# Kernel optimization log

Hardware: AMD Instinct MI355X
Metric: run time of the kernel (lower is better)

Reference implementation:

```python
import jax, jax.numpy as jnp
import numpy as np

H, W, DIM, B, K = 28, 28, 384, 64, 1
EPS = 1e-5


def setup_inputs() -> dict:
    key = jax.random.key(0)
    k1, k2, k3 = jax.random.split(key, 3)
    L = 1 + K * H * W
    x = jax.random.normal(k1, (B, L, DIM), dtype=jnp.float32)
    w_reduction = jax.random.normal(k2, (2 * DIM, 4 * DIM), dtype=jnp.float32) * 0.02
    w_convert = jax.random.normal(k3, (2 * DIM, DIM), dtype=jnp.float32) * 0.02
    ln_gamma = jnp.ones((4 * DIM,), dtype=jnp.float32)
    ln_beta = jnp.zeros((4 * DIM,), dtype=jnp.float32)
    return {"x": x, "w_reduction": w_reduction, "w_convert": w_convert,
            "ln_gamma": ln_gamma, "ln_beta": ln_beta}


def reference(x, w_reduction, w_convert, ln_gamma, ln_beta):
    Bb, L, C = x.shape
    k = (L - 1) // (H * W)
    cls_token = x[:, 0:1, :]                      # [B,1,C]
    feat = x[:, 1:, :].reshape(Bb, k, H, W, C)
    x0 = feat[:, :, 0::2, 0::2, :]                # [B,k,H/2,W/2,C]
    x1 = feat[:, :, 1::2, 0::2, :]
    x2 = feat[:, :, 0::2, 1::2, :]
    x3 = feat[:, :, 1::2, 1::2, :]
    m = jnp.concatenate([x0, x1, x2, x3], axis=-1)  # [B,k,H/2,W/2,4C]
    m = m.reshape(Bb, k, -1, 4 * C)
    # LayerNorm over last dim
    mu = jnp.mean(m, axis=-1, keepdims=True)
    var = jnp.mean(jnp.square(m - mu), axis=-1, keepdims=True)
    m = (m - mu) * jax.lax.rsqrt(var + EPS) * ln_gamma + ln_beta
    red = jnp.einsum('bknf,of->bkno', m, w_reduction).reshape(Bb, -1, 2 * C)
    cls_out = jnp.einsum('bic,oc->bio', cls_token, w_convert)  # [B,1,2C]
    return jnp.concatenate([cls_out, red], axis=1)
```

## Files before the change

### kernel.cpp

```cpp
#include <hip/hip_runtime.h>
#include <hip/hip_bf16.h>

#define DIMC 384
#define LL 785
#define FDIM 1536
#define ODIM 768
#define NPATCH 196
#define MROWS 12544
#define BATCH 64

typedef __attribute__((ext_vector_type(8))) short bf16x8;
typedef __attribute__((ext_vector_type(4))) float floatx4;
typedef __attribute__((ext_vector_type(4))) unsigned short ushort4v;

#define WS_WBF_OFF  38535168
#define WS_PST_OFF  40894464
#define WS_B2_OFF   41295872

#define PB_CLS   0
#define PB_CAST  192
#define PB_BIAS  1760
#define PB_WBF   1952
#define PREP_BLOCKS 3104

__device__ __forceinline__ unsigned short f2bf(float f) {
  union { float f; unsigned int u; } v; v.f = f;
  unsigned int u = v.u + 0x7fffu + ((v.u >> 16) & 1u);
  return (unsigned short)(u >> 16);
}

__device__ __forceinline__ void gload_lds16(const void* g, void* l) {
  __builtin_amdgcn_global_load_lds(
      (const __attribute__((address_space(1))) unsigned int*)g,
      (__attribute__((address_space(3))) unsigned int*)l, 16, 0, 0);
}

__global__ __launch_bounds__(256) void prep_kernel(
    const float* __restrict__ x, const float* __restrict__ wred,
    const float* __restrict__ wconv, const float* __restrict__ gamma,
    const float* __restrict__ beta, unsigned short* __restrict__ xbf,
    unsigned short* __restrict__ wbf, float2* __restrict__ pst,
    float2* __restrict__ bias2, float* __restrict__ out) {
  const int blk = blockIdx.x;
  const int t = threadIdx.x;
  const int wv = t >> 6;
  const int lane = t & 63;

  if (blk >= PB_CAST && blk < PB_BIAS) {
    const int w = (blk - PB_CAST) * 4 + wv;
    const int vid0 = w * 8 + (lane >> 4) * 2;
    const int sub = lane & 15;
    float4 v[2][6];
    float s[2], s2[2];
#pragma unroll
    for (int r = 0; r < 2; ++r) {
      int vid = vid0 + r;
      int b = vid / 784;
      int ll = vid - b * 784;
      const float* src = x + ((size_t)b * LL + 1 + ll) * DIMC;
      s[r] = 0.f; s2[r] = 0.f;
#pragma unroll
      for (int c = 0; c < 6; ++c) {
        float4 vv = *reinterpret_cast<const float4*>(src + sub * 4 + c * 64);
        v[r][c] = vv;
        s[r]  += vv.x + vv.y + vv.z + vv.w;
        s2[r] += vv.x * vv.x + vv.y * vv.y + vv.z * vv.z + vv.w * vv.w;
      }
    }
#pragma unroll
    for (int r = 0; r < 2; ++r) {
      unsigned short* dst = xbf + (size_t)(vid0 + r) * DIMC;
#pragma unroll
      for (int c = 0; c < 6; ++c) {
        float4 vv = v[r][c];
        union { ushort4v u4; __hip_bfloat162 h[2]; } u;
        u.h[0] = __float22bfloat162_rn(make_float2(vv.x, vv.y));
        u.h[1] = __float22bfloat162_rn(make_float2(vv.z, vv.w));
        *reinterpret_cast<ushort4v*>(dst + sub * 4 + c * 64) = u.u4;
      }
    }
#pragma unroll
    for (int o = 1; o < 16; o <<= 1) {
#pragma unroll
      for (int r = 0; r < 2; ++r) {
        s[r]  += __shfl_xor(s[r], o);
        s2[r] += __shfl_xor(s2[r], o);
      }
    }
    if (sub == 0) {
      float4 pp = make_float4(s[0], s2[0], s[1], s2[1]);
      *reinterpret_cast<float4*>(&pst[vid0]) = pp;
    }
  } else if (blk < PB_CAST) {
    __shared__ float xs[DIMC];
    int idx = blk;
    int b = idx / 3;
    int ch = idx - b * 3;
    for (int c = t; c < DIMC; c += 256) xs[c] = x[(size_t)b * LL * DIMC + c];
    __syncthreads();
    int o = ch * 256 + t;
    const float* wr = wconv + (size_t)o * DIMC;
    float a0 = 0.f, a1 = 0.f;
#pragma unroll 4
    for (int c = 0; c < DIMC; c += 8) {
      float4 w0 = *reinterpret_cast<const float4*>(wr + c);
      float4 w1 = *reinterpret_cast<const float4*>(wr + c + 4);
      float4 p0 = *reinterpret_cast<const float4*>(&xs[c]);
      float4 p1 = *reinterpret_cast<const float4*>(&xs[c + 4]);
      a0 += w0.x * p0.x + w0.y * p0.y + w0.z * p0.z + w0.w * p0.w;
      a1 += w1.x * p1.x + w1.y * p1.y + w1.z * p1.z + w1.w * p1.w;
    }
    out[(size_t)b * 197 * ODIM + o] = a0 + a1;
  } else if (blk < PB_WBF) {
    int o = (blk - PB_BIAS) * 4 + wv;
    const float* wr = wred + (size_t)o * FDIM;
    float sb = 0.f, sg = 0.f;
#pragma unroll
    for (int c = 0; c < 6; ++c) {
      int f = lane * 4 + c * 256;
      float4 w = *reinterpret_cast<const float4*>(wr + f);
      float4 be = *reinterpret_cast<const float4*>(beta + f);
      float4 ga = *reinterpret_cast<const float4*>(gamma + f);
      sb += w.x * be.x + w.y * be.y + w.z * be.z + w.w * be.w;
      sg += w.x * ga.x + w.y * ga.y + w.z * ga.z + w.w * ga.w;
    }
#pragma unroll
    for (int o2 = 32; o2 > 0; o2 >>= 1) {
      sb += __shfl_down(sb, o2);
      sg += __shfl_down(sg, o2);
    }
    if (lane == 0) bias2[o] = make_float2(sg, sb);
  } else {
    int idx4 = (blk - PB_WBF) * 256 + t;
    int e0 = idx4 * 4;
    int f = e0 % FDIM;
    float4 w = *reinterpret_cast<const float4*>(wred + e0);
    float4 g = *reinterpret_cast<const float4*>(gamma + f);
    ushort4v u;
    u.x = f2bf(w.x * g.x); u.y = f2bf(w.y * g.y);
    u.z = f2bf(w.z * g.z); u.w = f2bf(w.w * g.w);
    *reinterpret_cast<ushort4v*>(wbf + e0) = u;
  }
}

__global__ __launch_bounds__(256) void gemm_kernel(
    const unsigned short* __restrict__ xbf,
    const unsigned short* __restrict__ wbf,
    const float2* __restrict__ pst, const float2* __restrict__ bias2,
    float* __restrict__ out) {
  __shared__ unsigned short As[2][64 * 64];
  __shared__ unsigned short Bs[2][64 * 64];
  __shared__ float2 st[128];

  const int t = threadIdx.x;

  const int NWG = (ODIM / 128) * (MROWS / 128);
  const int qq = NWG >> 3, rr = NWG & 7;
  int bid = blockIdx.x;
  int xcd = bid & 7, pos = bid >> 3;
  int wg = (xcd < rr) ? xcd * (qq + 1) + pos
                      : rr * (qq + 1) + (xcd - rr) * qq + pos;
  int my = wg / 6;
  int nx = wg - my * 6;
  const int mBase = my * 128;
  const int nBase = nx * 128;

  if (t < 128) {
    int m = mBase + t;
    int b = m / NPATCH;
    int n = m - b * NPATCH;
    int i = n / 14;
    int j = n - i * 14;
    int base = b * 784 + i * 56 + j * 2;
    float2 p0 = pst[base];
    float2 p1 = pst[base + 28];
    float2 p2 = pst[base + 1];
    float2 p3 = pst[base + 29];
    float s = p0.x + p1.x + p2.x + p3.x;
    float s2 = p0.y + p1.y + p2.y + p3.y;
    float mu = s * (1.f / FDIM);
    float var = s2 * (1.f / FDIM) - mu * mu;
    float rs = rsqrtf(var + 1e-5f);
    st[t] = make_float2(rs, -mu * rs);
  }

  const unsigned short* agp[2];
  const unsigned short* bgp[2];
  unsigned int ldso[2];
#pragma unroll
  for (int p = 0; p < 2; ++p) {
    int s = p * 256 + t;
    int rho = s >> 3;
    int g = (s & 7) ^ (rho & 7);
    int r = rho + ((g >> 2) << 6);
    int kc = g & 3;
    int m = mBase + r;
    int b = m / NPATCH;
    int n = m - b * NPATCH;
    int i = n / 14;
    int j = n - i * 14;
    agp[p] = xbf + ((size_t)b * 784 + i * 56 + j * 2) * DIMC + kc * 8;
    bgp[p] = wbf + (size_t)(nBase + r) * FDIM + kc * 8;
    ldso[p] = (unsigned)s * 8;
  }

  const int wv = t >> 6;
  const int lane = t & 63;
  const int ln15 = lane & 15;
  const int quad = lane >> 4;
  const int wm = wv >> 1;
  const int wn = wv & 1;

  unsigned int aoff[4], boff[4];
#pragma unroll
  for (int mt = 0; mt < 4; ++mt) {
    int rho = mt * 16 + ln15;
    aoff[mt] = (unsigned)(rho * 64 + (((wm * 4 + quad) ^ (rho & 7)) * 8));
    boff[mt] = (unsigned)(rho * 64 + (((wn * 4 + quad) ^ (rho & 7)) * 8));
  }

  floatx4 acc[4][4];
#pragma unroll
  for (int mt = 0; mt < 4; ++mt)
#pragma unroll
    for (int nt = 0; nt < 4; ++nt)
      acc[mt][nt] = floatx4{0.f, 0.f, 0.f, 0.f};

#pragma unroll
  for (int p = 0; p < 2; ++p) {
    gload_lds16(agp[p], &As[0][ldso[p]]);
    gload_lds16(bgp[p], &Bs[0][ldso[p]]);
  }
  __syncthreads();

  int nq = 0, nkk = 0;
  for (int kt = 0; kt < FDIM / 32; ++kt) {
    const int cur = kt & 1;
    if (kt + 1 < FDIM / 32) {
      if (++nkk == 12) { nkk = 0; ++nq; }
      int ao = ((nq & 1) * 28 + ((nq >> 1) & 1)) * DIMC + nkk * 32;
#pragma unroll
      for (int p = 0; p < 2; ++p) {
        gload_lds16(agp[p] + ao, &As[cur ^ 1][ldso[p]]);
        bgp[p] += 32;
        gload_lds16(bgp[p], &Bs[cur ^ 1][ldso[p]]);
      }
    }
    bf16x8 af[4], bfr[4];
#pragma unroll
    for (int mt = 0; mt < 4; ++mt)
      af[mt] = *reinterpret_cast<const bf16x8*>(&As[cur][aoff[mt]]);
#pragma unroll
    for (int nt = 0; nt < 4; ++nt)
      bfr[nt] = *reinterpret_cast<const bf16x8*>(&Bs[cur][boff[nt]]);
#pragma unroll
    for (int mt = 0; mt < 4; ++mt)
#pragma unroll
      for (int nt = 0; nt < 4; ++nt)
        acc[mt][nt] = __builtin_amdgcn_mfma_f32_16x16x32_bf16(
            af[mt], bfr[nt], acc[mt][nt], 0, 0, 0);
    __syncthreads();
  }

  float2 gb[4];
#pragma unroll
  for (int nt = 0; nt < 4; ++nt)
    gb[nt] = bias2[nBase + wn * 64 + nt * 16 + ln15];
#pragma unroll
  for (int mt = 0; mt < 4; ++mt) {
#pragma unroll
    for (int r = 0; r < 4; ++r) {
      int rloc = wm * 64 + mt * 16 + quad * 4 + r;
      float2 sn = st[rloc];
      int m = mBase + rloc;
      int b = m / NPATCH;
      int n = m - b * NPATCH;
      float* orow = out + ((size_t)b * 197 + 1 + n) * ODIM + nBase + wn * 64;
#pragma unroll
      for (int nt = 0; nt < 4; ++nt) {
        float val = fmaf(acc[mt][nt][r], sn.x,
                         fmaf(sn.y, gb[nt].x, gb[nt].y));
        __builtin_nontemporal_store(val, &orow[nt * 16 + ln15]);
      }
    }
  }
}

extern "C" void kernel_launch(void* const* d_in, const int* in_sizes, int n_in,
                              void* d_out, int out_size, void* d_ws, size_t ws_size,
                              hipStream_t stream) {
  const float* x     = (const float*)d_in[0];
  const float* wred  = (const float*)d_in[1];
  const float* wconv = (const float*)d_in[2];
  const float* gamma = (const float*)d_in[3];
  const float* beta  = (const float*)d_in[4];
  float* out = (float*)d_out;

  unsigned short* xbf = (unsigned short*)d_ws;
  unsigned short* wbf = (unsigned short*)((char*)d_ws + WS_WBF_OFF);
  float2* pst         = (float2*)((char*)d_ws + WS_PST_OFF);
  float2* bias2       = (float2*)((char*)d_ws + WS_B2_OFF);

  prep_kernel<<<dim3(PREP_BLOCKS), 256, 0, stream>>>(x, wred, wconv, gamma,
                                                     beta, xbf, wbf, pst,
                                                     bias2, out);
  gemm_kernel<<<dim3((ODIM / 128) * (MROWS / 128)), 256, 0, stream>>>(
      xbf, wbf, pst, bias2, out);
}
```

Measured before the change: 196.6 us.

## Load GEMM weight fragments directly to registers and deepen K-step to 64

The weight (B) operand is no longer staged through shared memory. Each lane now loads its MFMA B fragments straight from global memory into registers, double-buffered across K steps. The A tile in LDS is enlarged to a 128x64 K-slice, which halves the number of K iterations and barriers. This removes the B-side LDS traffic and half of the synchronisation, at the cost of more VGPRs for the register-held B fragments and less coalesced global reads for the weights.

```diff
diff --git a/kernel.cpp b/kernel.cpp
--- a/kernel.cpp
+++ b/kernel.cpp
@@ -148,8 +148,7 @@
     const unsigned short* __restrict__ wbf,
     const float2* __restrict__ pst, const float2* __restrict__ bias2,
     float* __restrict__ out) {
-  __shared__ unsigned short As[2][64 * 64];
-  __shared__ unsigned short Bs[2][64 * 64];
+  __shared__ unsigned short As[2][128 * 64];
   __shared__ float2 st[128];
 
   const int t = threadIdx.x;
@@ -184,23 +183,19 @@
     st[t] = make_float2(rs, -mu * rs);
   }
 
-  const unsigned short* agp[2];
-  const unsigned short* bgp[2];
-  unsigned int ldso[2];
-#pragma unroll
-  for (int p = 0; p < 2; ++p) {
+  const unsigned short* agp[4];
+  unsigned int ldso[4];
+#pragma unroll
+  for (int p = 0; p < 4; ++p) {
     int s = p * 256 + t;
-    int rho = s >> 3;
-    int g = (s & 7) ^ (rho & 7);
-    int r = rho + ((g >> 2) << 6);
-    int kc = g & 3;
+    int r = s >> 3;
+    int cs = (s & 7) ^ (r & 7);
     int m = mBase + r;
     int b = m / NPATCH;
     int n = m - b * NPATCH;
     int i = n / 14;
     int j = n - i * 14;
-    agp[p] = xbf + ((size_t)b * 784 + i * 56 + j * 2) * DIMC + kc * 8;
-    bgp[p] = wbf + (size_t)(nBase + r) * FDIM + kc * 8;
+    agp[p] = xbf + ((size_t)b * 784 + i * 56 + j * 2) * DIMC + cs * 8;
     ldso[p] = (unsigned)s * 8;
   }
 
@@ -211,13 +206,20 @@
   const int wm = wv >> 1;
   const int wn = wv & 1;
 
-  unsigned int aoff[4], boff[4];
-#pragma unroll
-  for (int mt = 0; mt < 4; ++mt) {
-    int rho = mt * 16 + ln15;
-    aoff[mt] = (unsigned)(rho * 64 + (((wm * 4 + quad) ^ (rho & 7)) * 8));
-    boff[mt] = (unsigned)(rho * 64 + (((wn * 4 + quad) ^ (rho & 7)) * 8));
-  }
+  unsigned int aoff[4][2];
+#pragma unroll
+  for (int mt = 0; mt < 4; ++mt)
+#pragma unroll
+    for (int h = 0; h < 2; ++h) {
+      int rA = wm * 64 + mt * 16 + ln15;
+      aoff[mt][h] = (unsigned)(rA * 64 + (((h * 4 + quad) ^ (rA & 7)) * 8));
+    }
+
+  const unsigned short* bbase[4];
+#pragma unroll
+  for (int nt = 0; nt < 4; ++nt)
+    bbase[nt] = wbf + (size_t)(nBase + wn * 64 + nt * 16 + ln15) * FDIM
+              + quad * 8;
 
   floatx4 acc[4][4];
 #pragma unroll
@@ -226,40 +228,57 @@
     for (int nt = 0; nt < 4; ++nt)
       acc[mt][nt] = floatx4{0.f, 0.f, 0.f, 0.f};
 
-#pragma unroll
-  for (int p = 0; p < 2; ++p) {
-    gload_lds16(agp[p], &As[0][ldso[p]]);
-    gload_lds16(bgp[p], &Bs[0][ldso[p]]);
-  }
+  bf16x8 bA[8], bB[8];
+
+#pragma unroll
+  for (int p = 0; p < 4; ++p) gload_lds16(agp[p], &As[0][ldso[p]]);
+#pragma unroll
+  for (int nt = 0; nt < 4; ++nt)
+#pragma unroll
+    for (int h = 0; h < 2; ++h)
+      bA[nt * 2 + h] = *reinterpret_cast<const bf16x8*>(bbase[nt] + h * 32);
+#pragma unroll
+  for (int nt = 0; nt < 4; ++nt) bbase[nt] += 64;
   __syncthreads();
 
-  int nq = 0, nkk = 0;
-  for (int kt = 0; kt < FDIM / 32; ++kt) {
+  auto kstep = [&](int kt, bf16x8* Buse, bf16x8* Bpre) {
     const int cur = kt & 1;
-    if (kt + 1 < FDIM / 32) {
-      if (++nkk == 12) { nkk = 0; ++nq; }
-      int ao = ((nq & 1) * 28 + ((nq >> 1) & 1)) * DIMC + nkk * 32;
-#pragma unroll
-      for (int p = 0; p < 2; ++p) {
+    if (kt + 1 < FDIM / 64) {
+      int ktn = kt + 1;
+      int q = ktn / 6;
+      int kk = ktn - q * 6;
+      int ao = ((q & 1) * 28 + ((q >> 1) & 1)) * DIMC + kk * 64;
+#pragma unroll
+      for (int p = 0; p < 4; ++p)
         gload_lds16(agp[p] + ao, &As[cur ^ 1][ldso[p]]);
-        bgp[p] += 32;
-        gload_lds16(bgp[p], &Bs[cur ^ 1][ldso[p]]);
-      }
-    }
-    bf16x8 af[4], bfr[4];
-#pragma unroll
-    for (int mt = 0; mt < 4; ++mt)
-      af[mt] = *reinterpret_cast<const bf16x8*>(&As[cur][aoff[mt]]);
-#pragma unroll
-    for (int nt = 0; nt < 4; ++nt)
-      bfr[nt] = *reinterpret_cast<const bf16x8*>(&Bs[cur][boff[nt]]);
-#pragma unroll
-    for (int mt = 0; mt < 4; ++mt)
-#pragma unroll
-      for (int nt = 0; nt < 4; ++nt)
-        acc[mt][nt] = __builtin_amdgcn_mfma_f32_16x16x32_bf16(
-            af[mt], bfr[nt], acc[mt][nt], 0, 0, 0);
+#pragma unroll
+      for (int nt = 0; nt < 4; ++nt) {
+#pragma unroll
+        for (int h = 0; h < 2; ++h)
+          Bpre[nt * 2 + h] =
+              *reinterpret_cast<const bf16x8*>(bbase[nt] + h * 32);
+        bbase[nt] += 64;
+      }
+    }
+#pragma unroll
+    for (int h = 0; h < 2; ++h) {
+      bf16x8 af[4];
+#pragma unroll
+      for (int mt = 0; mt < 4; ++mt)
+        af[mt] = *reinterpret_cast<const bf16x8*>(&As[cur][aoff[mt][h]]);
+#pragma unroll
+      for (int mt = 0; mt < 4; ++mt)
+#pragma unroll
+        for (int nt = 0; nt < 4; ++nt)
+          acc[mt][nt] = __builtin_amdgcn_mfma_f32_16x16x32_bf16(
+              af[mt], Buse[nt * 2 + h], acc[mt][nt], 0, 0, 0);
+    }
     __syncthreads();
+  };
+
+  for (int kt2 = 0; kt2 < FDIM / 128; ++kt2) {
+    kstep(2 * kt2, bA, bB);
+    kstep(2 * kt2 + 1, bB, bA);
   }
 
   float2 gb[4];
```

Measured after the change: 223.3 us. 1.14x slower.
